# Kernel tuning notes

Hardware: AMD Instinct MI355X
Metric: run time of the kernel (lower is better)

The kernel has to match this reference:

```python
import jax, jax.numpy as jnp
import numpy as np

H = 16
MAX_REL = 128

def setup_inputs() -> dict:
    key = jax.random.key(0)
    ks = jax.random.split(key, 8)
    B, S, D = 4, 1024, 1024
    d_k = D // H
    return {
        "query": jax.random.normal(ks[0], (B, S, D), dtype=jnp.float32),
        "key": jax.random.normal(ks[1], (B, S, D), dtype=jnp.float32),
        "mask": jax.random.randint(ks[2], (B, S, S), 0, 2, dtype=jnp.int32),
        "Wq": jax.random.normal(ks[3], (D, D), dtype=jnp.float32) * 0.02,
        "bq": jax.random.normal(ks[4], (D,), dtype=jnp.float32) * 0.02,
        "Wk": jax.random.normal(ks[5], (D, D), dtype=jnp.float32) * 0.02,
        "bk": jax.random.normal(ks[6], (D,), dtype=jnp.float32) * 0.02,
        "rel_k_table": jax.random.normal(ks[7], (2 * MAX_REL + 1, d_k), dtype=jnp.float32) * 0.02,
    }

def reference(query, key, mask, Wq, bq, Wk, bk, rel_k_table):
    B, S, D = query.shape
    d_k = D // H
    scale = 1.0 / jnp.sqrt(jnp.asarray(d_k, dtype=query.dtype))
    # torch Linear: x @ W.T + b, then split heads -> [B, H, S, d_k]
    q = (query @ Wq.T + bq).reshape(B, S, H, d_k).transpose(0, 2, 1, 3)
    k = (key @ Wk.T + bk).reshape(B, S, H, d_k).transpose(0, 2, 1, 3)
    # relative position indices: clip(j - i, -P, P) + P  -> [S, S]
    pos = jnp.arange(S)
    rel_idx = jnp.clip(pos[None, :] - pos[:, None], -MAX_REL, MAX_REL) + MAX_REL
    rel_k = rel_k_table[rel_idx]  # [S, S, d_k]
    # content scores [B, H, S, S]
    scores = jnp.einsum('bhqd,bhkd->bhqk', q, k) * scale
    # relative bias: head-mean-pooled query vs per-(q,k) relative embedding -> [B, S, S]
    q_mean = q.mean(axis=1)  # [B, S, d_k]
    rel_scores = jnp.einsum('bqd,qkd->bqk', q_mean, rel_k) * scale
    scores = scores + rel_scores[:, None, :, :]
    # mask [B, S, S] -> [B, 1, S, S]; masked positions set to -1e9
    scores = jnp.where(mask[:, None, :, :] == 0, jnp.asarray(-1e9, scores.dtype), scores)
    return jax.nn.softmax(scores, axis=-1)  # [B, H, S, S]
```

## Files before the change

### kernel.cpp

```cpp
#include <hip/hip_runtime.h>
#include <hip/hip_bf16.h>

#define NP 257

typedef __attribute__((ext_vector_type(8))) short short8;
typedef __attribute__((ext_vector_type(4))) float f32x4;

__device__ __forceinline__ unsigned short f32_to_bf16(float f) {
    unsigned int u = __float_as_uint(f);
    unsigned int r = (u + 0x7FFFu + ((u >> 16) & 1u)) >> 16;
    return (unsigned short)r;
}
__device__ __forceinline__ float bf16_to_f32(unsigned short u) {
    return __uint_as_float(((unsigned int)u) << 16);
}
__device__ __forceinline__ float bf16_lo(unsigned int u) {
    return __uint_as_float(u << 16);
}
__device__ __forceinline__ float bf16_hi(unsigned int u) {
    return __uint_as_float(u & 0xFFFF0000u);
}

__global__ __launch_bounds__(256) void cvt_bf16_2(const float* __restrict__ s0,
                                                  unsigned short* __restrict__ d0,
                                                  const float* __restrict__ s1,
                                                  unsigned short* __restrict__ d1,
                                                  int n8)
{
    int i = blockIdx.x * 256 + threadIdx.x;
    if (i >= n8) return;
    const float* src = blockIdx.y ? s1 : s0;
    unsigned short* dst = blockIdx.y ? d1 : d0;
    const float4* s = reinterpret_cast<const float4*>(src) + (size_t)i * 2;
    float4 a = s[0], b = s[1];
    union { unsigned short u[8]; uint4 v; } p;
    p.u[0] = f32_to_bf16(a.x); p.u[1] = f32_to_bf16(a.y);
    p.u[2] = f32_to_bf16(a.z); p.u[3] = f32_to_bf16(a.w);
    p.u[4] = f32_to_bf16(b.x); p.u[5] = f32_to_bf16(b.y);
    p.u[6] = f32_to_bf16(b.z); p.u[7] = f32_to_bf16(b.w);
    reinterpret_cast<uint4*>(dst)[i] = p.v;
}

__global__ __launch_bounds__(256) void proj_mfma(const unsigned short* __restrict__ Xq,
                                                 const unsigned short* __restrict__ Wqb,
                                                 const float* __restrict__ bq,
                                                 unsigned short* __restrict__ outq,
                                                 const unsigned short* __restrict__ Xk,
                                                 const unsigned short* __restrict__ Wkb,
                                                 const float* __restrict__ bk,
                                                 unsigned short* __restrict__ outk)
{
    __shared__ unsigned short As[8192];
    __shared__ unsigned short Bs[8192];
    const unsigned short* Xb = blockIdx.z ? Xk : Xq;
    const unsigned short* Wb = blockIdx.z ? Wkb : Wqb;
    const float* bias        = blockIdx.z ? bk : bq;
    unsigned short* outb     = blockIdx.z ? outk : outq;

    const int tid = threadIdx.x;
    const int lane = tid & 63;
    const int w = tid >> 6;
    const int wi = w >> 1, wj = w & 1;
    const int bm = blockIdx.x * 128, bn = blockIdx.y * 128;
    const int r15 = lane & 15, g = lane >> 4;

    f32x4 acc[4][4];
    #pragma unroll
    for (int i = 0; i < 4; ++i)
        #pragma unroll
        for (int j = 0; j < 4; ++j) acc[i][j] = (f32x4){0.f, 0.f, 0.f, 0.f};

    size_t offA[4], offB[4];
    #pragma unroll
    for (int it = 0; it < 4; ++it) {
        int f = it * 256 + tid, row = f >> 3, cl = (f & 7) ^ (row & 7);
        offA[it] = (size_t)(bm + row) * 1024 + cl * 8;
        offB[it] = (size_t)(bn + row) * 1024 + cl * 8;
    }
    const int ldsbase = w * 512;

    for (int kt = 0; kt < 16; ++kt) {
        const int k0 = kt * 64;
        #pragma unroll
        for (int it = 0; it < 4; ++it)
            __builtin_amdgcn_global_load_lds(
                (const __attribute__((address_space(1))) void*)(Xb + offA[it] + k0),
                (__attribute__((address_space(3))) void*)(As + it * 2048 + ldsbase), 16, 0, 0);
        #pragma unroll
        for (int it = 0; it < 4; ++it)
            __builtin_amdgcn_global_load_lds(
                (const __attribute__((address_space(1))) void*)(Wb + offB[it] + k0),
                (__attribute__((address_space(3))) void*)(Bs + it * 2048 + ldsbase), 16, 0, 0);
        __syncthreads();

        #pragma unroll
        for (int kk = 0; kk < 2; ++kk) {
            const int c = kk * 4 + g;
            short8 a[4], bfr[4];
            #pragma unroll
            for (int ti = 0; ti < 4; ++ti) {
                const int ra = wi * 64 + ti * 16 + r15;
                a[ti] = *(const short8*)&As[(ra * 8 + (c ^ (ra & 7))) * 8];
            }
            #pragma unroll
            for (int tj = 0; tj < 4; ++tj) {
                const int rb = wj * 64 + tj * 16 + r15;
                bfr[tj] = *(const short8*)&Bs[(rb * 8 + (c ^ (rb & 7))) * 8];
            }
            #pragma unroll
            for (int ti = 0; ti < 4; ++ti)
                #pragma unroll
                for (int tj = 0; tj < 4; ++tj)
                    acc[ti][tj] = __builtin_amdgcn_mfma_f32_16x16x32_bf16(a[ti], bfr[tj], acc[ti][tj], 0, 0, 0);
        }
        __syncthreads();
    }

    #pragma unroll
    for (int tj = 0; tj < 4; ++tj) {
        const int n = bn + wj * 64 + tj * 16 + r15;
        const float bv = bias[n];
        #pragma unroll
        for (int ti = 0; ti < 4; ++ti) {
            const int orow = bm + wi * 64 + ti * 16 + (g << 2);
            #pragma unroll
            for (int r = 0; r < 4; ++r)
                outb[(size_t)(orow + r) * 1024 + n] = f32_to_bf16(acc[ti][tj][r] + bv);
        }
    }
}

__global__ __launch_bounds__(256) void biasrow(const unsigned short* __restrict__ qb,
                                               const float* __restrict__ relk,
                                               const int* __restrict__ mask,
                                               unsigned short* __restrict__ biasbf)
{
    __shared__ __align__(16) float qm[64];
    __shared__ float rd[NP];
    const int bi = blockIdx.x;
    const int i = bi & 1023;
    const int t = threadIdx.x;
    if (t < 64) {
        const unsigned short* qrow = qb + ((size_t)bi << 10);
        float s = 0.f;
        #pragma unroll
        for (int h2 = 0; h2 < 16; ++h2) s += bf16_to_f32(qrow[h2 * 64 + t]);
        qm[t] = s * 0.0625f;
    }
    __syncthreads();
    const float4* qm4 = reinterpret_cast<const float4*>(qm);
    for (int p = t; p < NP; p += 256) {
        const float4* rk4 = reinterpret_cast<const float4*>(relk + (size_t)p * 64);
        float s0 = 0.f, s1 = 0.f, s2 = 0.f, s3 = 0.f;
        #pragma unroll
        for (int d4 = 0; d4 < 16; ++d4) {
            float4 a = qm4[d4];
            float4 b = rk4[d4];
            s0 = fmaf(a.x, b.x, s0);
            s1 = fmaf(a.y, b.y, s1);
            s2 = fmaf(a.z, b.z, s2);
            s3 = fmaf(a.w, b.w, s3);
        }
        rd[p] = (s0 + s1 + s2 + s3) * 0.125f;
    }
    __syncthreads();

    const int4 mk = reinterpret_cast<const int4*>(mask + ((size_t)bi << 10))[t];
    const int j0 = t * 4;
    int d;
    float v0, v1, v2, v3;
    d = min(max(j0 + 0 - i, -128), 128); v0 = mk.x ? rd[d + 128] : -1e9f;
    d = min(max(j0 + 1 - i, -128), 128); v1 = mk.y ? rd[d + 128] : -1e9f;
    d = min(max(j0 + 2 - i, -128), 128); v2 = mk.z ? rd[d + 128] : -1e9f;
    d = min(max(j0 + 3 - i, -128), 128); v3 = mk.w ? rd[d + 128] : -1e9f;
    uint2 pk;
    pk.x = f32_to_bf16(v0) | ((unsigned int)f32_to_bf16(v1) << 16);
    pk.y = f32_to_bf16(v2) | ((unsigned int)f32_to_bf16(v3) << 16);
    *reinterpret_cast<uint2*>(biasbf + ((size_t)bi << 10) + j0) = pk;
}

__global__ __launch_bounds__(256) void attn5(const unsigned short* __restrict__ qb,
                                             const unsigned short* __restrict__ kb,
                                             const unsigned short* __restrict__ biasbf,
                                             float* __restrict__ out)
{
    __shared__ unsigned short e_lds[32 * 1024];
    __shared__ float redsum[4][32];
    const int i0 = blockIdx.x * 32;
    const int h = blockIdx.y, b = blockIdx.z;
    const int tid = threadIdx.x, lane = tid & 63, w = tid >> 6;
    const int r15 = lane & 15, g = lane >> 4;
    const size_t qkbase = ((size_t)b << 20) + h * 64;

    const unsigned short* qp0 = qb + qkbase + (size_t)(i0 + r15) * 1024 + 8 * g;
    const unsigned short* qp1 = qp0 + (16 << 10);
    short8 qf00 = *(const short8*)qp0,        qf01 = *(const short8*)(qp0 + 32);
    short8 qf10 = *(const short8*)qp1,        qf11 = *(const short8*)(qp1 + 32);

    const int ia = i0 + r15, ib = ia + 16;
    const unsigned short* bba = biasbf + (((size_t)(b * 1024 + ia)) << 10);
    const unsigned short* bbb = bba + (16 << 10);

    const int n0w = w * 256;
    float psA = 0.f, psB = 0.f;

    #pragma unroll 4
    for (int jt = 0; jt < 16; ++jt) {
        const int j0 = n0w + jt * 16;
        const unsigned short* kp = kb + qkbase + (size_t)(j0 + r15) * 1024 + 8 * g;
        short8 kf0 = *(const short8*)kp;
        short8 kf1 = *(const short8*)(kp + 32);
        f32x4 accA = (f32x4){0.f, 0.f, 0.f, 0.f};
        f32x4 accB = (f32x4){0.f, 0.f, 0.f, 0.f};
        accA = __builtin_amdgcn_mfma_f32_16x16x32_bf16(kf0, qf00, accA, 0, 0, 0);
        accB = __builtin_amdgcn_mfma_f32_16x16x32_bf16(kf0, qf10, accB, 0, 0, 0);
        accA = __builtin_amdgcn_mfma_f32_16x16x32_bf16(kf1, qf01, accA, 0, 0, 0);
        accB = __builtin_amdgcn_mfma_f32_16x16x32_bf16(kf1, qf11, accB, 0, 0, 0);

        const int jc = j0 + (g << 2);
        const uint2 bva = *reinterpret_cast<const uint2*>(bba + jc);
        const uint2 bvb = *reinterpret_cast<const uint2*>(bbb + jc);

        const float eA0 = __expf(fmaf(accA[0], 0.125f, bf16_lo(bva.x)));
        const float eA1 = __expf(fmaf(accA[1], 0.125f, bf16_hi(bva.x)));
        const float eA2 = __expf(fmaf(accA[2], 0.125f, bf16_lo(bva.y)));
        const float eA3 = __expf(fmaf(accA[3], 0.125f, bf16_hi(bva.y)));
        const float eB0 = __expf(fmaf(accB[0], 0.125f, bf16_lo(bvb.x)));
        const float eB1 = __expf(fmaf(accB[1], 0.125f, bf16_hi(bvb.x)));
        const float eB2 = __expf(fmaf(accB[2], 0.125f, bf16_lo(bvb.y)));
        const float eB3 = __expf(fmaf(accB[3], 0.125f, bf16_hi(bvb.y)));

        psA += (eA0 + eA1) + (eA2 + eA3);
        psB += (eB0 + eB1) + (eB2 + eB3);

        const unsigned int a0 = f32_to_bf16(eA0) | ((unsigned int)f32_to_bf16(eA1) << 16);
        const unsigned int a1 = f32_to_bf16(eA2) | ((unsigned int)f32_to_bf16(eA3) << 16);
        const unsigned int b0 = f32_to_bf16(eB0) | ((unsigned int)f32_to_bf16(eB1) << 16);
        const unsigned int b1 = f32_to_bf16(eB2) | ((unsigned int)f32_to_bf16(eB3) << 16);
        const int usA = r15 * 1024 + ((jc + r15 * 4) & 1023);
        const int usB = (16 + r15) * 1024 + ((jc + (16 + r15) * 4) & 1023);
        *reinterpret_cast<uint2*>(&e_lds[usA]) = make_uint2(a0, a1);
        *reinterpret_cast<uint2*>(&e_lds[usB]) = make_uint2(b0, b1);
    }

    psA += __shfl_xor(psA, 16, 64);
    psA += __shfl_xor(psA, 32, 64);
    psB += __shfl_xor(psB, 16, 64);
    psB += __shfl_xor(psB, 32, 64);
    if (lane < 16) {
        redsum[w][r15] = psA;
        redsum[w][16 + r15] = psB;
    }
    __syncthreads();

    #pragma unroll
    for (int rr8 = 0; rr8 < 8; ++rr8) {
        const int rl = w * 8 + rr8;
        const float inv = 1.0f / (redsum[0][rl] + redsum[1][rl] + redsum[2][rl] + redsum[3][rl]);
        float* op = out + (((size_t)((b * 16 + h) * 1024 + i0 + rl)) << 10);
        #pragma unroll
        for (int n = 0; n < 4; ++n) {
            const int c = n * 256 + lane * 4;
            const int us = rl * 1024 + ((c + rl * 4) & 1023);
            uint2 u = *reinterpret_cast<const uint2*>(&e_lds[us]);
            float4 v;
            v.x = bf16_to_f32((unsigned short)(u.x & 0xFFFFu)) * inv;
            v.y = bf16_to_f32((unsigned short)(u.x >> 16)) * inv;
            v.z = bf16_to_f32((unsigned short)(u.y & 0xFFFFu)) * inv;
            v.w = bf16_to_f32((unsigned short)(u.y >> 16)) * inv;
            *reinterpret_cast<float4*>(op + c) = v;
        }
    }
}

extern "C" void kernel_launch(void* const* d_in, const int* in_sizes, int n_in,
                              void* d_out, int out_size, void* d_ws, size_t ws_size,
                              hipStream_t stream) {
    const float* query = (const float*)d_in[0];
    const float* key   = (const float*)d_in[1];
    const int*   mask  = (const int*)d_in[2];
    const float* Wq    = (const float*)d_in[3];
    const float* bq    = (const float*)d_in[4];
    const float* Wk    = (const float*)d_in[5];
    const float* bk    = (const float*)d_in[6];
    const float* relk  = (const float*)d_in[7];

    char* ws = (char*)d_ws;
    unsigned short* qB     = (unsigned short*)(ws);
    unsigned short* kB     = (unsigned short*)(ws + (8u  << 20));
    unsigned short* queryb = (unsigned short*)(ws + (16u << 20));
    unsigned short* keyb   = (unsigned short*)(ws + (24u << 20));
    unsigned short* Wqb    = (unsigned short*)(ws + (32u << 20));
    unsigned short* Wkb    = (unsigned short*)(ws + (34u << 20));
    unsigned short* biasbf = (unsigned short*)(ws + (36u << 20));
    float*          out    = (float*)d_out;

    cvt_bf16_2<<<dim3(2048, 2), 256, 0, stream>>>(query, queryb, key, keyb, 524288);
    cvt_bf16_2<<<dim3(512, 2),  256, 0, stream>>>(Wq, Wqb, Wk, Wkb, 131072);

    proj_mfma<<<dim3(32, 8, 2), 256, 0, stream>>>(queryb, Wqb, bq, qB,
                                                  keyb,   Wkb, bk, kB);

    biasrow<<<4096, 256, 0, stream>>>(qB, relk, mask, biasbf);

    attn5<<<dim3(32, 16, 4), 256, 0, stream>>>(qB, kB, biasbf, out);
}
```

Before: 166.2 us.

## Double-buffer projection LDS tiles and shrink attention blocks to 16 rows with K prefetch

The projection GEMM gets double-buffered LDS so the global-to-LDS load for the next k-tile is issued before computing on the current one, with a single barrier per iteration. The attention kernel now handles 16 query rows per block instead of 32. This halves LDS use and doubles the grid, which should raise occupancy, and the head index moves to the fastest grid dimension so blocks sharing a bias row run close together. K fragments are register-prefetched one tile ahead, at the cost of twice the K reads per query row and fewer MFMAs per K load.

```diff
diff --git a/kernel.cpp b/kernel.cpp
--- a/kernel.cpp
+++ b/kernel.cpp
@@ -50,8 +50,8 @@
                                                  const float* __restrict__ bk,
                                                  unsigned short* __restrict__ outk)
 {
-    __shared__ unsigned short As[8192];
-    __shared__ unsigned short Bs[8192];
+    __shared__ unsigned short As[2][8192];
+    __shared__ unsigned short Bs[2][8192];
     const unsigned short* Xb = blockIdx.z ? Xk : Xq;
     const unsigned short* Wb = blockIdx.z ? Wkb : Wqb;
     const float* bias        = blockIdx.z ? bk : bq;
@@ -79,19 +79,26 @@
     }
     const int ldsbase = w * 512;
 
+#define PROJ_STAGE(buf, k0)                                                            \
+    {                                                                                  \
+        _Pragma("unroll")                                                              \
+        for (int it = 0; it < 4; ++it)                                                 \
+            __builtin_amdgcn_global_load_lds(                                          \
+                (const __attribute__((address_space(1))) void*)(Xb + offA[it] + (k0)), \
+                (__attribute__((address_space(3))) void*)(&As[buf][it * 2048 + ldsbase]), 16, 0, 0); \
+        _Pragma("unroll")                                                              \
+        for (int it = 0; it < 4; ++it)                                                 \
+            __builtin_amdgcn_global_load_lds(                                          \
+                (const __attribute__((address_space(1))) void*)(Wb + offB[it] + (k0)), \
+                (__attribute__((address_space(3))) void*)(&Bs[buf][it * 2048 + ldsbase]), 16, 0, 0); \
+    }
+
+    PROJ_STAGE(0, 0)
+    __syncthreads();
+
     for (int kt = 0; kt < 16; ++kt) {
-        const int k0 = kt * 64;
-        #pragma unroll
-        for (int it = 0; it < 4; ++it)
-            __builtin_amdgcn_global_load_lds(
-                (const __attribute__((address_space(1))) void*)(Xb + offA[it] + k0),
-                (__attribute__((address_space(3))) void*)(As + it * 2048 + ldsbase), 16, 0, 0);
-        #pragma unroll
-        for (int it = 0; it < 4; ++it)
-            __builtin_amdgcn_global_load_lds(
-                (const __attribute__((address_space(1))) void*)(Wb + offB[it] + k0),
-                (__attribute__((address_space(3))) void*)(Bs + it * 2048 + ldsbase), 16, 0, 0);
-        __syncthreads();
+        const int cur = kt & 1;
+        if (kt < 15) PROJ_STAGE(cur ^ 1, (kt + 1) * 64)
 
         #pragma unroll
         for (int kk = 0; kk < 2; ++kk) {
@@ -100,12 +107,12 @@
             #pragma unroll
             for (int ti = 0; ti < 4; ++ti) {
                 const int ra = wi * 64 + ti * 16 + r15;
-                a[ti] = *(const short8*)&As[(ra * 8 + (c ^ (ra & 7))) * 8];
+                a[ti] = *(const short8*)&As[cur][(ra * 8 + (c ^ (ra & 7))) * 8];
             }
             #pragma unroll
             for (int tj = 0; tj < 4; ++tj) {
                 const int rb = wj * 64 + tj * 16 + r15;
-                bfr[tj] = *(const short8*)&Bs[(rb * 8 + (c ^ (rb & 7))) * 8];
+                bfr[tj] = *(const short8*)&Bs[cur][(rb * 8 + (c ^ (rb & 7))) * 8];
             }
             #pragma unroll
             for (int ti = 0; ti < 4; ++ti)
@@ -115,6 +122,7 @@
         }
         __syncthreads();
     }
+#undef PROJ_STAGE
 
     #pragma unroll
     for (int tj = 0; tj < 4; ++tj) {
@@ -179,83 +187,71 @@
     *reinterpret_cast<uint2*>(biasbf + ((size_t)bi << 10) + j0) = pk;
 }
 
-__global__ __launch_bounds__(256) void attn5(const unsigned short* __restrict__ qb,
+__global__ __launch_bounds__(256) void attn6(const unsigned short* __restrict__ qb,
                                              const unsigned short* __restrict__ kb,
                                              const unsigned short* __restrict__ biasbf,
                                              float* __restrict__ out)
 {
-    __shared__ unsigned short e_lds[32 * 1024];
-    __shared__ float redsum[4][32];
-    const int i0 = blockIdx.x * 32;
-    const int h = blockIdx.y, b = blockIdx.z;
+    __shared__ unsigned short e_lds[16 * 1024];
+    __shared__ float redsum[4][16];
+    const int h = blockIdx.x;
+    const int i0 = blockIdx.y * 16;
+    const int b = blockIdx.z;
     const int tid = threadIdx.x, lane = tid & 63, w = tid >> 6;
     const int r15 = lane & 15, g = lane >> 4;
     const size_t qkbase = ((size_t)b << 20) + h * 64;
 
-    const unsigned short* qp0 = qb + qkbase + (size_t)(i0 + r15) * 1024 + 8 * g;
-    const unsigned short* qp1 = qp0 + (16 << 10);
-    short8 qf00 = *(const short8*)qp0,        qf01 = *(const short8*)(qp0 + 32);
-    short8 qf10 = *(const short8*)qp1,        qf11 = *(const short8*)(qp1 + 32);
-
-    const int ia = i0 + r15, ib = ia + 16;
+    const unsigned short* qp = qb + qkbase + (size_t)(i0 + r15) * 1024 + 8 * g;
+    short8 qf0 = *(const short8*)qp;
+    short8 qf1 = *(const short8*)(qp + 32);
+
+    const int ia = i0 + r15;
     const unsigned short* bba = biasbf + (((size_t)(b * 1024 + ia)) << 10);
-    const unsigned short* bbb = bba + (16 << 10);
-
     const int n0w = w * 256;
-    float psA = 0.f, psB = 0.f;
+    const unsigned short* kbase = kb + qkbase + (size_t)(n0w + r15) * 1024 + 8 * g;
+
+    float ps = 0.f;
+
+    short8 kc0 = *(const short8*)kbase;
+    short8 kc1 = *(const short8*)(kbase + 32);
 
     #pragma unroll 4
     for (int jt = 0; jt < 16; ++jt) {
-        const int j0 = n0w + jt * 16;
-        const unsigned short* kp = kb + qkbase + (size_t)(j0 + r15) * 1024 + 8 * g;
-        short8 kf0 = *(const short8*)kp;
-        short8 kf1 = *(const short8*)(kp + 32);
-        f32x4 accA = (f32x4){0.f, 0.f, 0.f, 0.f};
-        f32x4 accB = (f32x4){0.f, 0.f, 0.f, 0.f};
-        accA = __builtin_amdgcn_mfma_f32_16x16x32_bf16(kf0, qf00, accA, 0, 0, 0);
-        accB = __builtin_amdgcn_mfma_f32_16x16x32_bf16(kf0, qf10, accB, 0, 0, 0);
-        accA = __builtin_amdgcn_mfma_f32_16x16x32_bf16(kf1, qf01, accA, 0, 0, 0);
-        accB = __builtin_amdgcn_mfma_f32_16x16x32_bf16(kf1, qf11, accB, 0, 0, 0);
-
-        const int jc = j0 + (g << 2);
-        const uint2 bva = *reinterpret_cast<const uint2*>(bba + jc);
-        const uint2 bvb = *reinterpret_cast<const uint2*>(bbb + jc);
-
-        const float eA0 = __expf(fmaf(accA[0], 0.125f, bf16_lo(bva.x)));
-        const float eA1 = __expf(fmaf(accA[1], 0.125f, bf16_hi(bva.x)));
-        const float eA2 = __expf(fmaf(accA[2], 0.125f, bf16_lo(bva.y)));
-        const float eA3 = __expf(fmaf(accA[3], 0.125f, bf16_hi(bva.y)));
-        const float eB0 = __expf(fmaf(accB[0], 0.125f, bf16_lo(bvb.x)));
-        const float eB1 = __expf(fmaf(accB[1], 0.125f, bf16_hi(bvb.x)));
-        const float eB2 = __expf(fmaf(accB[2], 0.125f, bf16_lo(bvb.y)));
-        const float eB3 = __expf(fmaf(accB[3], 0.125f, bf16_hi(bvb.y)));
-
-        psA += (eA0 + eA1) + (eA2 + eA3);
-        psB += (eB0 + eB1) + (eB2 + eB3);
-
-        const unsigned int a0 = f32_to_bf16(eA0) | ((unsigned int)f32_to_bf16(eA1) << 16);
-        const unsigned int a1 = f32_to_bf16(eA2) | ((unsigned int)f32_to_bf16(eA3) << 16);
-        const unsigned int b0 = f32_to_bf16(eB0) | ((unsigned int)f32_to_bf16(eB1) << 16);
-        const unsigned int b1 = f32_to_bf16(eB2) | ((unsigned int)f32_to_bf16(eB3) << 16);
-        const int usA = r15 * 1024 + ((jc + r15 * 4) & 1023);
-        const int usB = (16 + r15) * 1024 + ((jc + (16 + r15) * 4) & 1023);
-        *reinterpret_cast<uint2*>(&e_lds[usA]) = make_uint2(a0, a1);
-        *reinterpret_cast<uint2*>(&e_lds[usB]) = make_uint2(b0, b1);
-    }
-
-    psA += __shfl_xor(psA, 16, 64);
-    psA += __shfl_xor(psA, 32, 64);
-    psB += __shfl_xor(psB, 16, 64);
-    psB += __shfl_xor(psB, 32, 64);
-    if (lane < 16) {
-        redsum[w][r15] = psA;
-        redsum[w][16 + r15] = psB;
-    }
+        short8 kn0, kn1;
+        if (jt < 15) {
+            const unsigned short* kp = kbase + (size_t)((jt + 1) * 16) * 1024;
+            kn0 = *(const short8*)kp;
+            kn1 = *(const short8*)(kp + 32);
+        }
+        f32x4 acc = (f32x4){0.f, 0.f, 0.f, 0.f};
+        acc = __builtin_amdgcn_mfma_f32_16x16x32_bf16(kc0, qf0, acc, 0, 0, 0);
+        acc = __builtin_amdgcn_mfma_f32_16x16x32_bf16(kc1, qf1, acc, 0, 0, 0);
+
+        const int jc = n0w + jt * 16 + (g << 2);
+        const uint2 bv = *reinterpret_cast<const uint2*>(bba + jc);
+        const float e0 = __expf(fmaf(acc[0], 0.125f, bf16_lo(bv.x)));
+        const float e1 = __expf(fmaf(acc[1], 0.125f, bf16_hi(bv.x)));
+        const float e2 = __expf(fmaf(acc[2], 0.125f, bf16_lo(bv.y)));
+        const float e3 = __expf(fmaf(acc[3], 0.125f, bf16_hi(bv.y)));
+        ps += (e0 + e1) + (e2 + e3);
+
+        const unsigned int u0 = f32_to_bf16(e0) | ((unsigned int)f32_to_bf16(e1) << 16);
+        const unsigned int u1 = f32_to_bf16(e2) | ((unsigned int)f32_to_bf16(e3) << 16);
+        const int us = r15 * 1024 + ((jc + r15 * 4) & 1023);
+        *reinterpret_cast<uint2*>(&e_lds[us]) = make_uint2(u0, u1);
+
+        kc0 = kn0;
+        kc1 = kn1;
+    }
+
+    ps += __shfl_xor(ps, 16, 64);
+    ps += __shfl_xor(ps, 32, 64);
+    if (lane < 16) redsum[w][r15] = ps;
     __syncthreads();
 
     #pragma unroll
-    for (int rr8 = 0; rr8 < 8; ++rr8) {
-        const int rl = w * 8 + rr8;
+    for (int rr = 0; rr < 4; ++rr) {
+        const int rl = w * 4 + rr;
         const float inv = 1.0f / (redsum[0][rl] + redsum[1][rl] + redsum[2][rl] + redsum[3][rl]);
         float* op = out + (((size_t)((b * 16 + h) * 1024 + i0 + rl)) << 10);
         #pragma unroll
@@ -303,5 +299,5 @@
 
     biasrow<<<4096, 256, 0, stream>>>(qB, relk, mask, biasbf);
 
-    attn5<<<dim3(32, 16, 4), 256, 0, stream>>>(qB, kB, biasbf, out);
-}
+    attn6<<<dim3(16, 64, 4), 256, 0, stream>>>(qB, kB, biasbf, out);
+}
```

New measurement: 190.6 us. 1.15x slower.
